# Kernel tuning notes

Hardware: AMD Instinct MI355X
Metric: run time of the kernel (lower is better)

## Reference

```python
import jax, jax.numpy as jnp
import numpy as np

NUM_HEADS = 16
N_EMBED = 1024
HEAD_SIZE = 64
BLOCK_SIZE = 2048


def setup_inputs() -> dict:
    key = jax.random.key(0)
    ks = jax.random.split(key, 6)
    B, S, C, H, D = 2, BLOCK_SIZE, N_EMBED, NUM_HEADS, HEAD_SIZE
    x = jax.random.normal(ks[0], (B, S, C), dtype=jnp.float32)
    scale = C ** -0.5
    # per-head q/k/v projections (bias=False), stacked over heads: [H, C, D]
    Wq = jax.random.normal(ks[1], (H, C, D), dtype=jnp.float32) * scale
    Wk = jax.random.normal(ks[2], (H, C, D), dtype=jnp.float32) * scale
    Wv = jax.random.normal(ks[3], (H, C, D), dtype=jnp.float32) * scale
    # output projection Linear(H*D, C)
    Wo = jax.random.normal(ks[4], (H * D, C), dtype=jnp.float32) * ((H * D) ** -0.5)
    bo = jax.random.normal(ks[5], (C,), dtype=jnp.float32) * 0.01
    return {"x": x, "Wq": Wq, "Wk": Wk, "Wv": Wv, "Wo": Wo, "bo": bo}


def reference(x, Wq, Wk, Wv, Wo, bo):
    B, S, C = x.shape
    H, _, D = Wq.shape
    # project: [B, H, S, D]
    q = jnp.einsum("bsc,hcd->bhsd", x, Wq)
    k = jnp.einsum("bsc,hcd->bhsd", x, Wk)
    v = jnp.einsum("bsc,hcd->bhsd", x, Wv)
    # scaled causal attention scores: [B, H, S, S]
    scores = jnp.einsum("bhsd,bhtd->bhst", q, k) * (D ** -0.5)
    causal = jnp.tril(jnp.ones((S, S), dtype=bool))
    scores = jnp.where(causal, scores, jnp.finfo(scores.dtype).min)
    attn = jax.nn.softmax(scores, axis=-1)
    out = jnp.einsum("bhst,bhtd->bhsd", attn, v)  # [B, H, S, D]
    # concat heads -> [B, S, H*D], then output projection
    out = out.transpose(0, 2, 1, 3).reshape(B, S, H * D)
    return out @ Wo + bo
```

## Files before the change

kernel.cpp:

```cpp
#include <hip/hip_runtime.h>
#include <cstdint>
#include <cstddef>

constexpr int SEQ  = 2048;
constexpr int CH   = 1024;
constexpr int NH   = 16;
constexpr int HS   = 64;
constexpr int NB   = 2;
constexpr int HDIM = NH * HS;

typedef __bf16 bf16x8 __attribute__((ext_vector_type(8)));
typedef __bf16 bf16x4 __attribute__((ext_vector_type(4)));
typedef float  f32x4  __attribute__((ext_vector_type(4)));

__device__ __forceinline__ unsigned short f2bf(float f) {
  union { float f; unsigned u; } v; v.f = f;
  unsigned u = v.u;
  u += 0x7fffu + ((u >> 16) & 1u);
  return (unsigned short)(u >> 16);
}
__device__ __forceinline__ float bf2f(unsigned short h) {
  union { unsigned u; float f; } v; v.u = ((unsigned)h) << 16;
  return v.f;
}
__device__ __forceinline__ float load_elem(const void* p, int flag, size_t idx) {
  if (flag) return ((const float*)p)[idx];
  return bf2f(((const unsigned short*)p)[idx]);
}
__device__ __forceinline__ void gl_lds16(const unsigned short* g, unsigned short* l) {
  __builtin_amdgcn_global_load_lds(
      (const __attribute__((address_space(1))) unsigned int*)g,
      (__attribute__((address_space(3))) unsigned int*)l, 16, 0, 0);
}

__device__ int detect_flag_block(const void* p, int n, int tid, int nthr) {
  __shared__ int det_good;
  if (tid == 0) det_good = 0;
  __syncthreads();
  const unsigned short* u = (const unsigned short*)p;
  int good = 0;
  for (int j = tid; j < n; j += nthr) {
    unsigned short v = u[2 * j];
    int e = (v >> 7) & 0xFF;
    if (v != 0 && e >= 90 && e <= 150) good++;
  }
  atomicAdd(&det_good, good);
  __syncthreads();
  return (det_good * 10 >= n * 7) ? 0 : 1;
}

__global__ __launch_bounds__(256) void prep(
    const void* __restrict__ x,  const void* __restrict__ wq,
    const void* __restrict__ wk, const void* __restrict__ wv,
    const void* __restrict__ wo,
    unsigned short* __restrict__ xb,
    unsigned short* __restrict__ wall,
    unsigned short* __restrict__ wot) {
  __shared__ unsigned short tile[32][33];
  int idx = blockIdx.x, tid = threadIdx.x;
  if (idx < 1024) {
    int f = detect_flag_block(x, 512, tid, 256);
    size_t n4 = (size_t)NB * SEQ * CH / 4;
    for (size_t i = (size_t)idx * 256 + tid; i < n4; i += (size_t)1024 * 256) {
      ushort4 o;
      if (f) {
        float4 v = ((const float4*)x)[i];
        o.x = f2bf(v.x); o.y = f2bf(v.y); o.z = f2bf(v.z); o.w = f2bf(v.w);
      } else {
        o = ((const ushort4*)x)[i];
      }
      ((ushort4*)xb)[i] = o;
    }
  } else if (idx < 4096) {
    int j = idx - 1024;
    int which = j >> 10, hh = (j >> 6) & 15, sub = j & 63;
    const void* src = (which == 0) ? wq : (which == 1) ? wk : wv;
    int f = detect_flag_block(src, 512, tid, 256);
    int c0 = (sub & 1) * 32;
    int r0 = (sub >> 1) * 32;
    int tx = tid & 31, ty = tid >> 5;
    size_t boff = (size_t)hh * CH * HS;
    for (int i = ty; i < 32; i += 8)
      tile[i][tx] = f2bf(load_elem(src, f, boff + (size_t)(r0 + i) * HS + c0 + tx));
    __syncthreads();
    unsigned short* d = wall + ((size_t)which * NH + hh) * HS * CH;
    for (int i = ty; i < 32; i += 8)
      d[(size_t)(c0 + i) * CH + r0 + tx] = tile[tx][i];
  } else {
    int sub = idx - 4096;
    int f = detect_flag_block(wo, 512, tid, 256);
    int c0 = (sub & 31) * 32;
    int r0 = (sub >> 5) * 32;
    int tx = tid & 31, ty = tid >> 5;
    for (int i = ty; i < 32; i += 8)
      tile[i][tx] = f2bf(load_elem(wo, f, (size_t)(r0 + i) * CH + c0 + tx));
    __syncthreads();
    for (int i = ty; i < 32; i += 8)
      wot[(size_t)(c0 + i) * HDIM + r0 + tx] = tile[tx][i];
  }
}

__global__ __launch_bounds__(256) void qkv_gemm(
    const unsigned short* __restrict__ xb,
    const unsigned short* __restrict__ wall,
    unsigned short* __restrict__ qo,
    unsigned short* __restrict__ ko,
    unsigned short* __restrict__ vt) {
  __shared__ __attribute__((aligned(16))) unsigned short Al[128 * 64];
  __shared__ __attribute__((aligned(16))) unsigned short Bl[128 * 64];
  int mt = blockIdx.x, nt = blockIdx.y;
  const unsigned short* A  = xb   + (size_t)mt * 128 * CH;
  const unsigned short* Bm = wall + (size_t)nt * 128 * CH;
  int tid = threadIdx.x, wave = tid >> 6, lane = tid & 63;
  int quad = lane >> 4, l15 = lane & 15;
  int r8 = lane >> 3, c8 = lane & 7;
  int gcol = ((c8 ^ r8) << 3);
  int x7 = l15 & 7;
  int wm = (wave >> 1) * 64, wn = (wave & 1) * 64;
  f32x4 acc[4][4];
  #pragma unroll
  for (int i = 0; i < 4; i++)
    #pragma unroll
    for (int j = 0; j < 4; j++) acc[i][j] = (f32x4){0.f, 0.f, 0.f, 0.f};

  for (int k0 = 0; k0 < CH; k0 += 64) {
    #pragma unroll
    for (int c = 0; c < 4; c++) {
      int row = wave * 32 + c * 8 + r8;
      gl_lds16(&A [(size_t)row * CH + k0 + gcol], &Al[(wave * 32 + c * 8) * 64]);
      gl_lds16(&Bm[(size_t)row * CH + k0 + gcol], &Bl[(wave * 32 + c * 8) * 64]);
    }
    __syncthreads();
    #pragma unroll
    for (int h = 0; h < 2; h++) {
      int cq = ((quad + 4 * h) ^ x7) << 3;
      bf16x8 af[4], bfr[4];
      #pragma unroll
      for (int fm = 0; fm < 4; fm++)
        af[fm] = *reinterpret_cast<const bf16x8*>(&Al[(wm + fm * 16 + l15) * 64 + cq]);
      #pragma unroll
      for (int fn = 0; fn < 4; fn++)
        bfr[fn] = *reinterpret_cast<const bf16x8*>(&Bl[(wn + fn * 16 + l15) * 64 + cq]);
      #pragma unroll
      for (int fm = 0; fm < 4; fm++)
        #pragma unroll
        for (int fn = 0; fn < 4; fn++)
          acc[fm][fn] = __builtin_amdgcn_mfma_f32_16x16x32_bf16(af[fm], bfr[fn], acc[fm][fn], 0, 0, 0);
    }
    __syncthreads();
  }

  int seg = (nt * 128) >> 10;
  int nb  = (nt * 128) & 1023;
  if (seg < 2) {
    unsigned short* dst = (seg == 0) ? qo : ko;
    float s = (seg == 0) ? 0.18033688011112042f : 1.0f;
    #pragma unroll
    for (int fn = 0; fn < 4; fn++) {
      int c = nb + wn + fn * 16 + l15, h = c >> 6, d = c & 63;
      #pragma unroll
      for (int fm = 0; fm < 4; fm++) {
        int m = mt * 128 + wm + fm * 16 + quad * 4;
        int b = m >> 11, s0 = m & 2047;
        #pragma unroll
        for (int r = 0; r < 4; r++)
          dst[(((size_t)b * NH + h) * SEQ + s0 + r) * HS + d] = f2bf(acc[fm][fn][r] * s);
      }
    }
  } else {
    #pragma unroll
    for (int fn = 0; fn < 4; fn++) {
      int c = nb + wn + fn * 16 + l15, h = c >> 6, d = c & 63;
      #pragma unroll
      for (int fm = 0; fm < 4; fm++) {
        int m = mt * 128 + wm + fm * 16 + quad * 4;
        int b = m >> 11, s0 = m & 2047;
        ushort4 pk;
        pk.x = f2bf(acc[fm][fn][0]); pk.y = f2bf(acc[fm][fn][1]);
        pk.z = f2bf(acc[fm][fn][2]); pk.w = f2bf(acc[fm][fn][3]);
        *(ushort4*)&vt[(((size_t)b * NH + h) * HS + d) * SEQ + s0] = pk;
      }
    }
  }
}

template <bool MASKED>
__device__ __forceinline__ void soft_pack(const f32x4* s, f32x4& ls,
                                          unsigned short* ptRow, int quad, int tmb) {
  #pragma unroll
  for (int tb = 0; tb < 4; tb++) {
    f32x4 pv;
    #pragma unroll
    for (int r = 0; r < 4; r++) {
      float p = __builtin_amdgcn_exp2f(s[tb][r]);
      if (MASKED) { if (tmb + tb * 16 + quad * 4 + r > 0) p = 0.f; }
      pv[r] = p;
    }
    ls += pv;
    bf16x4 pk;
    pk.x = (__bf16)pv[0]; pk.y = (__bf16)pv[1];
    pk.z = (__bf16)pv[2]; pk.w = (__bf16)pv[3];
    *(bf16x4*)&ptRow[tb * 16 + quad * 4] = pk;
  }
}

template <int MODE>
__device__ __forceinline__ void attn_tile(
    const unsigned short (&Kb)[64][64], const unsigned short (&Vb)[64][64],
    unsigned short* p0row, unsigned short* p1row,
    const bf16x8 (&qf)[2][2], f32x4 (&lsum)[2], f32x4 (&accO)[2][4],
    int quad, int l15, int tmb) {
  constexpr bool C0 = (MODE <= 1);
  constexpr bool M0 = (MODE == 1);
  constexpr bool M1 = (MODE == 3);
  int x7 = l15 & 7;
  f32x4 s0[4], s1[4];
  #pragma unroll
  for (int tb = 0; tb < 4; tb++) { s0[tb] = (f32x4){0,0,0,0}; s1[tb] = (f32x4){0,0,0,0}; }
  __builtin_amdgcn_s_setprio(1);
  #pragma unroll
  for (int tb = 0; tb < 4; tb++)
    #pragma unroll
    for (int hh = 0; hh < 2; hh++) {
      bf16x8 kf = *reinterpret_cast<const bf16x8*>(
          &Kb[tb * 16 + l15][((hh * 4 + quad) ^ x7) << 3]);
      if (C0) s0[tb] = __builtin_amdgcn_mfma_f32_16x16x32_bf16(kf, qf[0][hh], s0[tb], 0, 0, 0);
      s1[tb] = __builtin_amdgcn_mfma_f32_16x16x32_bf16(kf, qf[1][hh], s1[tb], 0, 0, 0);
    }
  __builtin_amdgcn_s_setprio(0);
  if (C0) soft_pack<M0>(s0, lsum[0], p0row, quad, tmb);
  soft_pack<M1>(s1, lsum[1], p1row, quad, tmb);

  bf16x8 bq0[2], bq1[2];
  #pragma unroll
  for (int tp = 0; tp < 2; tp++) {
    if (C0) bq0[tp] = *reinterpret_cast<const bf16x8*>(&p0row[tp * 32 + quad * 8]);
    bq1[tp] = *reinterpret_cast<const bf16x8*>(&p1row[tp * 32 + quad * 8]);
  }
  __builtin_amdgcn_s_setprio(1);
  #pragma unroll
  for (int db = 0; db < 4; db++)
    #pragma unroll
    for (int tp = 0; tp < 2; tp++) {
      bf16x8 vf = *reinterpret_cast<const bf16x8*>(
          &Vb[db * 16 + l15][((tp * 4 + quad) ^ x7) << 3]);
      if (C0) accO[0][db] = __builtin_amdgcn_mfma_f32_16x16x32_bf16(vf, bq0[tp], accO[0][db], 0, 0, 0);
      accO[1][db] = __builtin_amdgcn_mfma_f32_16x16x32_bf16(vf, bq1[tp], accO[1][db], 0, 0, 0);
    }
  __builtin_amdgcn_s_setprio(0);
}

__global__ __launch_bounds__(256) void attn_k(
    const unsigned short* __restrict__ q,
    const unsigned short* __restrict__ k,
    const unsigned short* __restrict__ vt,
    unsigned short* __restrict__ y) {
  __shared__ __attribute__((aligned(16))) unsigned short Kl[2][64][64];
  __shared__ __attribute__((aligned(16))) unsigned short Vl[2][64][64];
  __shared__ __attribute__((aligned(16))) unsigned short Pt[4][16][152];

  int p = blockIdx.x;
  int st0 = p, st1 = 31 - p;
  int bh = blockIdx.y, b = bh >> 4, h = bh & 15;
  const unsigned short* Q0 = q + ((size_t)bh * SEQ + st0 * 64) * HS;
  const unsigned short* Q1 = q + ((size_t)bh * SEQ + st1 * 64) * HS;
  const unsigned short* K  = k  + (size_t)bh * SEQ * HS;
  const unsigned short* V  = vt + (size_t)bh * HS * SEQ;
  int tid = threadIdx.x, wave = tid >> 6, lane = tid & 63;
  int quad = lane >> 4, l15 = lane & 15;
  int lr = tid >> 3, lc = (tid & 7) * 8;
  int sc = (((tid & 7) ^ (lr & 7)) << 3);

  bf16x8 qf[2][2];
  #pragma unroll
  for (int hh = 0; hh < 2; hh++) {
    qf[0][hh] = *reinterpret_cast<const bf16x8*>(
        &Q0[(size_t)(wave * 16 + l15) * HS + hh * 32 + quad * 8]);
    qf[1][hh] = *reinterpret_cast<const bf16x8*>(
        &Q1[(size_t)(wave * 16 + l15) * HS + hh * 32 + quad * 8]);
  }

  f32x4 lsum[2] = {(f32x4){0,0,0,0}, (f32x4){0,0,0,0}};
  f32x4 accO[2][4];
  #pragma unroll
  for (int f = 0; f < 2; f++)
    #pragma unroll
    for (int i = 0; i < 4; i++) accO[f][i] = (f32x4){0.f, 0.f, 0.f, 0.f};

  unsigned short* p0row = &Pt[wave][l15][0];
  unsigned short* p1row = &Pt[wave][l15][64];
  int tmb = -(wave * 16 + l15);

  uint4 kr0, kr1, vr0, vr1;
  auto g2r = [&](int kv) {
    kr0 = *(const uint4*)&K[(size_t)(kv * 64 + lr) * HS + lc];
    kr1 = *(const uint4*)&K[(size_t)(kv * 64 + lr + 32) * HS + lc];
    vr0 = *(const uint4*)&V[(size_t)lr * SEQ + kv * 64 + lc];
    vr1 = *(const uint4*)&V[(size_t)(lr + 32) * SEQ + kv * 64 + lc];
  };
  auto r2l = [&](int nb) {
    *(uint4*)&Kl[nb][lr][sc] = kr0; *(uint4*)&Kl[nb][lr + 32][sc] = kr1;
    *(uint4*)&Vl[nb][lr][sc] = vr0; *(uint4*)&Vl[nb][lr + 32][sc] = vr1;
  };

  int last = st1;
  g2r(0); r2l(0);
  __syncthreads();
  for (int kv = 0; kv <= last; kv++) {
    int cb = kv & 1;
    if (kv < last) g2r(kv + 1);
    if (kv < st0)
      attn_tile<0>(Kl[cb], Vl[cb], p0row, p1row, qf, lsum, accO, quad, l15, tmb);
    else if (kv == st0)
      attn_tile<1>(Kl[cb], Vl[cb], p0row, p1row, qf, lsum, accO, quad, l15, tmb);
    else if (kv < st1)
      attn_tile<2>(Kl[cb], Vl[cb], p0row, p1row, qf, lsum, accO, quad, l15, tmb);
    else
      attn_tile<3>(Kl[cb], Vl[cb], p0row, p1row, qf, lsum, accO, quad, l15, tmb);
    if (kv < last) r2l(cb ^ 1);
    __syncthreads();
  }

  #pragma unroll
  for (int f = 0; f < 2; f++) {
    float rs = (lsum[f][0] + lsum[f][1]) + (lsum[f][2] + lsum[f][3]);
    rs += __shfl_xor(rs, 16); rs += __shfl_xor(rs, 32);
    float inv = 1.0f / fmaxf(rs, 1e-30f);
    int srow = (f == 0 ? st0 : st1) * 64 + wave * 16 + l15;
    #pragma unroll
    for (int db = 0; db < 4; db++) {
      ushort4 pk;
      pk.x = f2bf(accO[f][db][0] * inv); pk.y = f2bf(accO[f][db][1] * inv);
      pk.z = f2bf(accO[f][db][2] * inv); pk.w = f2bf(accO[f][db][3] * inv);
      *(ushort4*)&y[((size_t)b * SEQ + srow) * HDIM + h * 64 + db * 16 + quad * 4] = pk;
    }
  }
}

__global__ __launch_bounds__(256) void out_gemm(
    const unsigned short* __restrict__ y,
    const unsigned short* __restrict__ wot,
    const void* __restrict__ bo,
    float* __restrict__ out) {
  __shared__ __attribute__((aligned(16))) unsigned short Al[128 * 64];
  __shared__ __attribute__((aligned(16))) unsigned short Bl[128 * 64];
  int tid = threadIdx.x;
  int fbo = detect_flag_block(bo, 512, tid, 256);
  int mt = blockIdx.x, nt = blockIdx.y;
  const unsigned short* A  = y   + (size_t)mt * 128 * HDIM;
  const unsigned short* Bm = wot + (size_t)nt * 128 * HDIM;
  int wave = tid >> 6, lane = tid & 63;
  int quad = lane >> 4, l15 = lane & 15;
  int r8 = lane >> 3, c8 = lane & 7;
  int gcol = ((c8 ^ r8) << 3);
  int x7 = l15 & 7;
  int wm = (wave >> 1) * 64, wn = (wave & 1) * 64;
  f32x4 acc[4][4];
  #pragma unroll
  for (int i = 0; i < 4; i++)
    #pragma unroll
    for (int j = 0; j < 4; j++) acc[i][j] = (f32x4){0.f, 0.f, 0.f, 0.f};

  for (int k0 = 0; k0 < HDIM; k0 += 64) {
    #pragma unroll
    for (int c = 0; c < 4; c++) {
      int row = wave * 32 + c * 8 + r8;
      gl_lds16(&A [(size_t)row * HDIM + k0 + gcol], &Al[(wave * 32 + c * 8) * 64]);
      gl_lds16(&Bm[(size_t)row * HDIM + k0 + gcol], &Bl[(wave * 32 + c * 8) * 64]);
    }
    __syncthreads();
    #pragma unroll
    for (int h = 0; h < 2; h++) {
      int cq = ((quad + 4 * h) ^ x7) << 3;
      bf16x8 af[4], bfr[4];
      #pragma unroll
      for (int fm = 0; fm < 4; fm++)
        af[fm] = *reinterpret_cast<const bf16x8*>(&Al[(wm + fm * 16 + l15) * 64 + cq]);
      #pragma unroll
      for (int fn = 0; fn < 4; fn++)
        bfr[fn] = *reinterpret_cast<const bf16x8*>(&Bl[(wn + fn * 16 + l15) * 64 + cq]);
      #pragma unroll
      for (int fm = 0; fm < 4; fm++)
        #pragma unroll
        for (int fn = 0; fn < 4; fn++)
          acc[fm][fn] = __builtin_amdgcn_mfma_f32_16x16x32_bf16(af[fm], bfr[fn], acc[fm][fn], 0, 0, 0);
    }
    __syncthreads();
  }

  #pragma unroll
  for (int fn = 0; fn < 4; fn++) {
    int n = nt * 128 + wn + fn * 16 + l15;
    float bias = load_elem(bo, fbo, n);
    #pragma unroll
    for (int fm = 0; fm < 4; fm++) {
      int m = mt * 128 + wm + fm * 16 + quad * 4;
      #pragma unroll
      for (int r = 0; r < 4; r++)
        out[(size_t)(m + r) * CH + n] = acc[fm][fn][r] + bias;
    }
  }
}

extern "C" void kernel_launch(void* const* d_in, const int* in_sizes, int n_in,
                              void* d_out, int out_size, void* d_ws, size_t ws_size,
                              hipStream_t stream) {
  const void* x  = d_in[0];
  const void* Wq = d_in[1];
  const void* Wk = d_in[2];
  const void* Wv = d_in[3];
  const void* Wo = d_in[4];
  const void* bo = d_in[5];
  float* out = (float*)d_out;

  char* ws = (char*)d_ws;
  const size_t MB = 1024 * 1024;
  unsigned short* qb   = (unsigned short*)(ws + 0);
  unsigned short* kb   = (unsigned short*)(ws + 8  * MB);
  unsigned short* vtb  = (unsigned short*)(ws + 16 * MB);
  unsigned short* yb   = (unsigned short*)(ws + 24 * MB);
  unsigned short* wall = (unsigned short*)(ws + 32 * MB);
  unsigned short* wot  = (unsigned short*)(ws + 38 * MB);
  unsigned short* xb   = (unsigned short*)(ws + 40 * MB);

  prep<<<5120, 256, 0, stream>>>(x, Wq, Wk, Wv, Wo, xb, wall, wot);
  qkv_gemm<<<dim3(NB * SEQ / 128, 3 * HDIM / 128), 256, 0, stream>>>(xb, wall, qb, kb, vtb);
  attn_k<<<dim3(16, NB * NH), 256, 0, stream>>>(qb, kb, vtb, yb);
  out_gemm<<<dim3(NB * SEQ / 128, CH / 128), 256, 0, stream>>>(yb, wot, bo, out);
}
```

Measured before the change: 206.7 us.

## Software-pipeline attention PV with next QK, vectorize prep transposes, shrink out_gemm N tile

The attention loop is restructured so the P·V MFMAs of the previous tile are issued alongside the QK MFMAs of the current tile. A triple-buffered K/V LDS layout keeps the lagged V tile resident, and the last P·V is drained after the loop. The prep transposes now use 4-wide vector loads and stores through a padded tile, and out_gemm uses a 128x64 tile that doubles the block count for better CU occupancy. The changes add LDS usage and register pressure from the carried P fragments, and the control flow around the pipeline stages becomes more complex.

```diff
diff --git a/kernel.cpp b/kernel.cpp
--- a/kernel.cpp
+++ b/kernel.cpp
@@ -56,8 +56,10 @@
     unsigned short* __restrict__ xb,
     unsigned short* __restrict__ wall,
     unsigned short* __restrict__ wot) {
-  __shared__ unsigned short tile[32][33];
+  __shared__ unsigned short tile[32][36];
   int idx = blockIdx.x, tid = threadIdx.x;
+  int row = tid >> 3, cg = (tid & 7) * 4;
+  int col = tid >> 3, rg = (tid & 7) * 4;
   if (idx < 1024) {
     int f = detect_flag_block(x, 512, tid, 256);
     size_t n4 = (size_t)NB * SEQ * CH / 4;
@@ -78,25 +80,41 @@
     int f = detect_flag_block(src, 512, tid, 256);
     int c0 = (sub & 1) * 32;
     int r0 = (sub >> 1) * 32;
-    int tx = tid & 31, ty = tid >> 5;
     size_t boff = (size_t)hh * CH * HS;
-    for (int i = ty; i < 32; i += 8)
-      tile[i][tx] = f2bf(load_elem(src, f, boff + (size_t)(r0 + i) * HS + c0 + tx));
+    size_t si = boff + (size_t)(r0 + row) * HS + c0 + cg;
+    ushort4 t4;
+    if (f) {
+      float4 v = *(const float4*)((const float*)src + si);
+      t4.x = f2bf(v.x); t4.y = f2bf(v.y); t4.z = f2bf(v.z); t4.w = f2bf(v.w);
+    } else {
+      t4 = *(const ushort4*)((const unsigned short*)src + si);
+    }
+    *(ushort4*)&tile[row][cg] = t4;
     __syncthreads();
     unsigned short* d = wall + ((size_t)which * NH + hh) * HS * CH;
-    for (int i = ty; i < 32; i += 8)
-      d[(size_t)(c0 + i) * CH + r0 + tx] = tile[tx][i];
+    ushort4 o;
+    o.x = tile[rg + 0][col]; o.y = tile[rg + 1][col];
+    o.z = tile[rg + 2][col]; o.w = tile[rg + 3][col];
+    *(ushort4*)&d[(size_t)(c0 + col) * CH + r0 + rg] = o;
   } else {
     int sub = idx - 4096;
     int f = detect_flag_block(wo, 512, tid, 256);
     int c0 = (sub & 31) * 32;
     int r0 = (sub >> 5) * 32;
-    int tx = tid & 31, ty = tid >> 5;
-    for (int i = ty; i < 32; i += 8)
-      tile[i][tx] = f2bf(load_elem(wo, f, (size_t)(r0 + i) * CH + c0 + tx));
-    __syncthreads();
-    for (int i = ty; i < 32; i += 8)
-      wot[(size_t)(c0 + i) * HDIM + r0 + tx] = tile[tx][i];
+    size_t si = (size_t)(r0 + row) * CH + c0 + cg;
+    ushort4 t4;
+    if (f) {
+      float4 v = *(const float4*)((const float*)wo + si);
+      t4.x = f2bf(v.x); t4.y = f2bf(v.y); t4.z = f2bf(v.z); t4.w = f2bf(v.w);
+    } else {
+      t4 = *(const ushort4*)((const unsigned short*)wo + si);
+    }
+    *(ushort4*)&tile[row][cg] = t4;
+    __syncthreads();
+    ushort4 o;
+    o.x = tile[rg + 0][col]; o.y = tile[rg + 1][col];
+    o.z = tile[rg + 2][col]; o.w = tile[rg + 3][col];
+    *(ushort4*)&wot[(size_t)(c0 + col) * HDIM + r0 + rg] = o;
   }
 }
 
@@ -204,15 +222,16 @@
   }
 }
 
-template <int MODE>
-__device__ __forceinline__ void attn_tile(
-    const unsigned short (&Kb)[64][64], const unsigned short (&Vb)[64][64],
+template <int QKM, bool PV0, bool PVV>
+__device__ __forceinline__ void attn_step(
+    const unsigned short (&Kb)[64][64], const unsigned short (&Vp)[64][64],
     unsigned short* p0row, unsigned short* p1row,
     const bf16x8 (&qf)[2][2], f32x4 (&lsum)[2], f32x4 (&accO)[2][4],
+    bf16x8 (&bq0)[2], bf16x8 (&bq1)[2],
     int quad, int l15, int tmb) {
-  constexpr bool C0 = (MODE <= 1);
-  constexpr bool M0 = (MODE == 1);
-  constexpr bool M1 = (MODE == 3);
+  constexpr bool C0 = (QKM <= 1);
+  constexpr bool M0 = (QKM == 1);
+  constexpr bool M1 = (QKM == 3);
   int x7 = l15 & 7;
   f32x4 s0[4], s1[4];
   #pragma unroll
@@ -227,27 +246,25 @@
       if (C0) s0[tb] = __builtin_amdgcn_mfma_f32_16x16x32_bf16(kf, qf[0][hh], s0[tb], 0, 0, 0);
       s1[tb] = __builtin_amdgcn_mfma_f32_16x16x32_bf16(kf, qf[1][hh], s1[tb], 0, 0, 0);
     }
+  if (PVV) {
+    #pragma unroll
+    for (int db = 0; db < 4; db++)
+      #pragma unroll
+      for (int tp = 0; tp < 2; tp++) {
+        bf16x8 vf = *reinterpret_cast<const bf16x8*>(
+            &Vp[db * 16 + l15][((tp * 4 + quad) ^ x7) << 3]);
+        if (PV0) accO[0][db] = __builtin_amdgcn_mfma_f32_16x16x32_bf16(vf, bq0[tp], accO[0][db], 0, 0, 0);
+        accO[1][db] = __builtin_amdgcn_mfma_f32_16x16x32_bf16(vf, bq1[tp], accO[1][db], 0, 0, 0);
+      }
+  }
   __builtin_amdgcn_s_setprio(0);
   if (C0) soft_pack<M0>(s0, lsum[0], p0row, quad, tmb);
   soft_pack<M1>(s1, lsum[1], p1row, quad, tmb);
-
-  bf16x8 bq0[2], bq1[2];
   #pragma unroll
   for (int tp = 0; tp < 2; tp++) {
     if (C0) bq0[tp] = *reinterpret_cast<const bf16x8*>(&p0row[tp * 32 + quad * 8]);
     bq1[tp] = *reinterpret_cast<const bf16x8*>(&p1row[tp * 32 + quad * 8]);
   }
-  __builtin_amdgcn_s_setprio(1);
-  #pragma unroll
-  for (int db = 0; db < 4; db++)
-    #pragma unroll
-    for (int tp = 0; tp < 2; tp++) {
-      bf16x8 vf = *reinterpret_cast<const bf16x8*>(
-          &Vb[db * 16 + l15][((tp * 4 + quad) ^ x7) << 3]);
-      if (C0) accO[0][db] = __builtin_amdgcn_mfma_f32_16x16x32_bf16(vf, bq0[tp], accO[0][db], 0, 0, 0);
-      accO[1][db] = __builtin_amdgcn_mfma_f32_16x16x32_bf16(vf, bq1[tp], accO[1][db], 0, 0, 0);
-    }
-  __builtin_amdgcn_s_setprio(0);
 }
 
 __global__ __launch_bounds__(256) void attn_k(
@@ -255,8 +272,8 @@
     const unsigned short* __restrict__ k,
     const unsigned short* __restrict__ vt,
     unsigned short* __restrict__ y) {
-  __shared__ __attribute__((aligned(16))) unsigned short Kl[2][64][64];
-  __shared__ __attribute__((aligned(16))) unsigned short Vl[2][64][64];
+  __shared__ __attribute__((aligned(16))) unsigned short Kl[3][64][64];
+  __shared__ __attribute__((aligned(16))) unsigned short Vl[3][64][64];
   __shared__ __attribute__((aligned(16))) unsigned short Pt[4][16][152];
 
   int p = blockIdx.x;
@@ -286,6 +303,7 @@
   for (int f = 0; f < 2; f++)
     #pragma unroll
     for (int i = 0; i < 4; i++) accO[f][i] = (f32x4){0.f, 0.f, 0.f, 0.f};
+  bf16x8 bq0[2], bq1[2];
 
   unsigned short* p0row = &Pt[wave][l15][0];
   unsigned short* p1row = &Pt[wave][l15][64];
@@ -303,22 +321,63 @@
     *(uint4*)&Vl[nb][lr][sc] = vr0; *(uint4*)&Vl[nb][lr + 32][sc] = vr1;
   };
 
-  int last = st1;
   g2r(0); r2l(0);
   __syncthreads();
-  for (int kv = 0; kv <= last; kv++) {
-    int cb = kv & 1;
-    if (kv < last) g2r(kv + 1);
-    if (kv < st0)
-      attn_tile<0>(Kl[cb], Vl[cb], p0row, p1row, qf, lsum, accO, quad, l15, tmb);
-    else if (kv == st0)
-      attn_tile<1>(Kl[cb], Vl[cb], p0row, p1row, qf, lsum, accO, quad, l15, tmb);
-    else if (kv < st1)
-      attn_tile<2>(Kl[cb], Vl[cb], p0row, p1row, qf, lsum, accO, quad, l15, tmb);
+
+  {
+    if (st1 > 0) g2r(1);
+    if (st0 == 0)
+      attn_step<1, false, false>(Kl[0], Vl[2], p0row, p1row, qf, lsum, accO, bq0, bq1, quad, l15, tmb);
     else
-      attn_tile<3>(Kl[cb], Vl[cb], p0row, p1row, qf, lsum, accO, quad, l15, tmb);
-    if (kv < last) r2l(cb ^ 1);
-    __syncthreads();
+      attn_step<0, false, false>(Kl[0], Vl[2], p0row, p1row, qf, lsum, accO, bq0, bq1, quad, l15, tmb);
+    if (st1 > 0) r2l(1);
+    __syncthreads();
+  }
+  for (int t = 1; t < st0; t++) {
+    g2r(t + 1);
+    attn_step<0, true, true>(Kl[t % 3], Vl[(t + 2) % 3], p0row, p1row, qf, lsum, accO, bq0, bq1, quad, l15, tmb);
+    r2l((t + 1) % 3);
+    __syncthreads();
+  }
+  if (st0 >= 1) {
+    int t = st0;
+    g2r(t + 1);
+    attn_step<1, true, true>(Kl[t % 3], Vl[(t + 2) % 3], p0row, p1row, qf, lsum, accO, bq0, bq1, quad, l15, tmb);
+    r2l((t + 1) % 3);
+    __syncthreads();
+  }
+  {
+    int t = st0 + 1;
+    bool more = (t < st1);
+    if (more) g2r(t + 1);
+    if (t == st1)
+      attn_step<3, true, true>(Kl[t % 3], Vl[(t + 2) % 3], p0row, p1row, qf, lsum, accO, bq0, bq1, quad, l15, tmb);
+    else
+      attn_step<2, true, true>(Kl[t % 3], Vl[(t + 2) % 3], p0row, p1row, qf, lsum, accO, bq0, bq1, quad, l15, tmb);
+    if (more) r2l((t + 1) % 3);
+    __syncthreads();
+  }
+  for (int t = st0 + 2; t < st1; t++) {
+    g2r(t + 1);
+    attn_step<2, false, true>(Kl[t % 3], Vl[(t + 2) % 3], p0row, p1row, qf, lsum, accO, bq0, bq1, quad, l15, tmb);
+    r2l((t + 1) % 3);
+    __syncthreads();
+  }
+  if (st1 >= st0 + 2) {
+    int t = st1;
+    attn_step<3, false, true>(Kl[t % 3], Vl[(t + 2) % 3], p0row, p1row, qf, lsum, accO, bq0, bq1, quad, l15, tmb);
+  }
+  {
+    const unsigned short (&Vb)[64][64] = Vl[st1 % 3];
+    int x7 = l15 & 7;
+    #pragma unroll
+    for (int db = 0; db < 4; db++)
+      #pragma unroll
+      for (int tp = 0; tp < 2; tp++) {
+        bf16x8 vf = *reinterpret_cast<const bf16x8*>(
+            &Vb[db * 16 + l15][((tp * 4 + quad) ^ x7) << 3]);
+        accO[1][db] = __builtin_amdgcn_mfma_f32_16x16x32_bf16(vf, bq1[tp], accO[1][db], 0, 0, 0);
+      }
   }
 
   #pragma unroll
@@ -343,54 +402,58 @@
     const void* __restrict__ bo,
     float* __restrict__ out) {
   __shared__ __attribute__((aligned(16))) unsigned short Al[128 * 64];
-  __shared__ __attribute__((aligned(16))) unsigned short Bl[128 * 64];
+  __shared__ __attribute__((aligned(16))) unsigned short Bl[64 * 64];
   int tid = threadIdx.x;
   int fbo = detect_flag_block(bo, 512, tid, 256);
   int mt = blockIdx.x, nt = blockIdx.y;
   const unsigned short* A  = y   + (size_t)mt * 128 * HDIM;
-  const unsigned short* Bm = wot + (size_t)nt * 128 * HDIM;
+  const unsigned short* Bm = wot + (size_t)nt * 64 * HDIM;
   int wave = tid >> 6, lane = tid & 63;
   int quad = lane >> 4, l15 = lane & 15;
   int r8 = lane >> 3, c8 = lane & 7;
   int gcol = ((c8 ^ r8) << 3);
   int x7 = l15 & 7;
-  int wm = (wave >> 1) * 64, wn = (wave & 1) * 64;
-  f32x4 acc[4][4];
+  int wm = (wave >> 1) * 64, wn = (wave & 1) * 32;
+  f32x4 acc[4][2];
   #pragma unroll
   for (int i = 0; i < 4; i++)
     #pragma unroll
-    for (int j = 0; j < 4; j++) acc[i][j] = (f32x4){0.f, 0.f, 0.f, 0.f};
+    for (int j = 0; j < 2; j++) acc[i][j] = (f32x4){0.f, 0.f, 0.f, 0.f};
 
   for (int k0 = 0; k0 < HDIM; k0 += 64) {
     #pragma unroll
     for (int c = 0; c < 4; c++) {
       int row = wave * 32 + c * 8 + r8;
-      gl_lds16(&A [(size_t)row * HDIM + k0 + gcol], &Al[(wave * 32 + c * 8) * 64]);
-      gl_lds16(&Bm[(size_t)row * HDIM + k0 + gcol], &Bl[(wave * 32 + c * 8) * 64]);
+      gl_lds16(&A[(size_t)row * HDIM + k0 + gcol], &Al[(wave * 32 + c * 8) * 64]);
+    }
+    #pragma unroll
+    for (int c = 0; c < 2; c++) {
+      int row = wave * 16 + c * 8 + r8;
+      gl_lds16(&Bm[(size_t)row * HDIM + k0 + gcol], &Bl[(wave * 16 + c * 8) * 64]);
     }
     __syncthreads();
     #pragma unroll
     for (int h = 0; h < 2; h++) {
       int cq = ((quad + 4 * h) ^ x7) << 3;
-      bf16x8 af[4], bfr[4];
+      bf16x8 af[4], bfr[2];
       #pragma unroll
       for (int fm = 0; fm < 4; fm++)
         af[fm] = *reinterpret_cast<const bf16x8*>(&Al[(wm + fm * 16 + l15) * 64 + cq]);
       #pragma unroll
-      for (int fn = 0; fn < 4; fn++)
+      for (int fn = 0; fn < 2; fn++)
         bfr[fn] = *reinterpret_cast<const bf16x8*>(&Bl[(wn + fn * 16 + l15) * 64 + cq]);
       #pragma unroll
       for (int fm = 0; fm < 4; fm++)
         #pragma unroll
-        for (int fn = 0; fn < 4; fn++)
+        for (int fn = 0; fn < 2; fn++)
           acc[fm][fn] = __builtin_amdgcn_mfma_f32_16x16x32_bf16(af[fm], bfr[fn], acc[fm][fn], 0, 0, 0);
     }
     __syncthreads();
   }
 
   #pragma unroll
-  for (int fn = 0; fn < 4; fn++) {
-    int n = nt * 128 + wn + fn * 16 + l15;
+  for (int fn = 0; fn < 2; fn++) {
+    int n = nt * 64 + wn + fn * 16 + l15;
     float bias = load_elem(bo, fbo, n);
     #pragma unroll
     for (int fm = 0; fm < 4; fm++) {
@@ -426,5 +489,5 @@
   prep<<<5120, 256, 0, stream>>>(x, Wq, Wk, Wv, Wo, xb, wall, wot);
   qkv_gemm<<<dim3(NB * SEQ / 128, 3 * HDIM / 128), 256, 0, stream>>>(xb, wall, qb, kb, vtb);
   attn_k<<<dim3(16, NB * NH), 256, 0, stream>>>(qb, kb, vtb, yb);
-  out_gemm<<<dim3(NB * SEQ / 128, CH / 128), 256, 0, stream>>>(yb, wot, bo, out);
-}
+  out_gemm<<<dim3(NB * SEQ / 128, CH / 64), 256, 0, stream>>>(yb, wot, bo, out);
+}
```

After: 187.6 us. -9.2%, faster.
